# Kernel tuning notes

Hardware: AMD Instinct MI355X
Metric: run time of the kernel (lower is better)

Reference implementation:

```python
import jax, jax.numpy as jnp
import numpy as np

BLANK = 0
ALPHA = 0.25
GAMMA = 2.0
NEG = -1e30  # log-domain 'minus infinity' (finite to stay autodiff/bf16 safe)


def setup_inputs() -> dict:
    key = jax.random.key(0)
    k1, k2, k3 = jax.random.split(key, 3)
    B, T, C, S = 32, 512, 4000, 40
    tokens_btc = jax.random.normal(k1, (B, T, C), dtype=jnp.float32)
    targets_bxt = jax.random.randint(k2, (B, S), 1, C)            # labels exclude blank=0
    targets_lengths_bx1 = jax.random.randint(k3, (B,), 10, S + 1)  # per-sample target lengths
    return {
        "tokens_btc": tokens_btc,
        "targets_bxt": targets_bxt,
        "targets_lengths_bx1": targets_lengths_bx1,
    }


def _ctc_loss(log_probs_tbc, targets, target_lengths, blank):
    """Log-domain CTC forward (alpha) recursion; input lengths == T for all samples.
    Returns per-sample negative log likelihood, shape [B]."""
    T, B, C = log_probs_tbc.shape
    S = targets.shape[1]
    L = 2 * S + 1  # extended target: blank-interleaved
    ext = jnp.full((B, L), blank, dtype=targets.dtype).at[:, 1::2].set(targets)
    # skip transition (s-2 -> s) allowed iff ext[s] != blank and ext[s] != ext[s-2]
    same_as_2back = jnp.concatenate(
        [jnp.ones((B, 2), bool), ext[:, 2:] == ext[:, :-2]], axis=1)
    skip_ok = (ext != blank) & (~same_as_2back)  # [B, L]

    b_idx = jnp.arange(B)[:, None]
    lp_ext = log_probs_tbc[:, b_idx, ext]  # [T, B, L] gathered emission log-probs

    alpha0 = jnp.full((B, L), NEG, log_probs_tbc.dtype)
    alpha0 = alpha0.at[:, 0].set(lp_ext[0, :, 0]).at[:, 1].set(lp_ext[0, :, 1])

    pad1 = jnp.full((B, 1), NEG, log_probs_tbc.dtype)
    pad2 = jnp.full((B, 2), NEG, log_probs_tbc.dtype)

    def step(alpha, lp_t):
        s1 = jnp.concatenate([pad1, alpha[:, :-1]], axis=1)
        s2 = jnp.concatenate([pad2, alpha[:, :-2]], axis=1)
        a = jnp.logaddexp(alpha, s1)
        a = jnp.where(skip_ok, jnp.logaddexp(a, s2), a)
        return a + lp_t, None

    alphaT, _ = jax.lax.scan(step, alpha0, lp_ext[1:])
    end = 2 * target_lengths  # index of final blank in extended sequence
    a_last = jnp.take_along_axis(alphaT, end[:, None], axis=1)[:, 0]
    a_prev = jnp.take_along_axis(alphaT, (end - 1)[:, None], axis=1)[:, 0]
    loss = -jnp.logaddexp(a_last, a_prev)
    # zero_infinity=True: clamp infinite losses to 0
    return jnp.where(loss < 1e29, loss, 0.0)


def reference(tokens_btc, targets_bxt, targets_lengths_bx1):
    # [B,T,C] -> [T,B,C], log_softmax over classes
    log_probs_tbc = jax.nn.log_softmax(tokens_btc, axis=-1).swapaxes(0, 1)
    loss = _ctc_loss(log_probs_tbc, targets_bxt, targets_lengths_bx1, BLANK)
    # focal reweighting (alpha>0 and gamma>=0 -> enabled)
    pt = jnp.exp(-loss)
    loss = ALPHA * (1.0 - pt) ** GAMMA * loss
    return jnp.mean(loss)
```

## Files before the change

### kernel.cpp

```cpp
#include <hip/hip_runtime.h>


constexpr int B = 32;
constexpr int T = 512;
constexpr int C = 4000;
constexpr int S = 40;
constexpr int L = 2 * S + 1;
constexpr int LPS = 82;

constexpr int GATHER_BLOCKS = 1016;
constexpr int GW = GATHER_BLOCKS * 4;
constexpr int NBLK = GATHER_BLOCKS + 8;

#define NEGV -1e30f

__device__ __forceinline__ float lae(float a, float b) {
    float m = fmaxf(a, b);
    float d = fabsf(a - b);
    return m + __logf(1.0f + __expf(-d));
}

__device__ __forceinline__ float shr1_fill_neg(float x) {
    return __int_as_float(__builtin_amdgcn_update_dpp(
        __float_as_int(NEGV), __float_as_int(x),
        0x138 , 0xF, 0xF, false));
}

__global__ __launch_bounds__(256) void zero_flags_kernel(unsigned int* p, int n) {
    const int i = blockIdx.x * 256 + threadIdx.x;
    if (i < n) p[i] = 0u;
}

__global__ __launch_bounds__(256, 4) void fused_kernel(
        const float* __restrict__ tok,
        const int*   __restrict__ tgt,
        const int*   __restrict__ lens,
        float*       __restrict__ lp,
        unsigned char* __restrict__ flags,
        unsigned int* __restrict__ ctr,
        float*       __restrict__ loss_b,
        float*       __restrict__ out) {
    const int wave = threadIdx.x >> 6, lane = threadIdx.x & 63;

    if (blockIdx.x < GATHER_BLOCKS) {
        const int wg = blockIdx.x * 4 + wave;
        for (int rp = wg; rp < B * T; rp += GW) {
            const int t  = rp >> 5;
            const int bb = rp & 31;
            const int row = (bb << 9) + t;
            const size_t row_off = (size_t)row * C;
            const float4* row4 = (const float4*)(tok + row_off);

            float s = 0.0f;
            #pragma unroll
            for (int k = 0; k < 16; ++k) {
                const int i = lane + 64 * k;
                if (i < C / 4) {
                    float4 v = row4[i];
                    s += __expf(v.x) + __expf(v.y) + __expf(v.z) + __expf(v.w);
                }
            }
            #pragma unroll
            for (int off = 32; off; off >>= 1) s += __shfl_xor(s, off);
            const float lse = __logf(s);

            float* dst = lp + (size_t)row * LPS;
            {
                const int l = lane;
                int lab = 0;
                if (l & 1) lab = tgt[bb * S + (l >> 1)];
                __hip_atomic_store(dst + l, tok[row_off + lab] - lse,
                                   __ATOMIC_RELAXED, __HIP_MEMORY_SCOPE_AGENT);
            }
            if (lane < LPS - 64) {
                const int l = 64 + lane;
                float v = 0.0f;
                if (l < L) {
                    int lab = 0;
                    if (l & 1) lab = tgt[bb * S + (l >> 1)];
                    v = tok[row_off + lab] - lse;
                }
                __hip_atomic_store(dst + l, v,
                                   __ATOMIC_RELAXED, __HIP_MEMORY_SCOPE_AGENT);
            }
            asm volatile("s_waitcnt vmcnt(0)" ::: "memory");
            if (lane == 0)
                __hip_atomic_store(flags + row, (unsigned char)1,
                                   __ATOMIC_RELAXED, __HIP_MEMORY_SCOPE_AGENT);
        }
        return;
    }

    const int b  = ((blockIdx.x - GATHER_BLOCKS) << 2) + wave;
    const int ii = (lane < 41) ? lane : 40;
    const float2* base2 = (const float2*)(lp + (size_t)b * T * LPS);
    unsigned long long* fw = (unsigned long long*)(flags + ((size_t)b << 9));
    const unsigned long long ONESW = 0x0101010101010101ull;

    int ti = tgt[b * S + ((ii < 39) ? ii : 39)];
    int tp = __shfl_up(ti, 1);
    const bool skip1 = (lane >= 1) && (lane <= 39) && (ti != tp);
    const int len = lens[b];

    float a0, a1;
    auto step = [&](float2 v) {
        float p1 = shr1_fill_neg(a1);
        float m0 = fmaxf(a0, p1);
        float n0 = m0 + __logf(__expf(a0 - m0) + __expf(p1 - m0));
        float q  = skip1 ? p1 : NEGV;
        float m1 = fmaxf(fmaxf(a1, a0), q);
        float n1 = m1 + __logf(__expf(a1 - m1) + __expf(a0 - m1) + __expf(q - m1));
        a0 = n0 + v.x;
        a1 = n1 + v.y;
    };

    float2 bufA[8], bufB[8];
    unsigned long long pf = 0;

#define SPINCHUNK(c) do {                                                     \
        while (pf != ONESW)                                                   \
            pf = __hip_atomic_load(&fw[(c)], __ATOMIC_RELAXED,                \
                                   __HIP_MEMORY_SCOPE_AGENT);                 \
        __builtin_amdgcn_fence(__ATOMIC_ACQUIRE, "agent");                    \
    } while (0)
#define PREFETCHF(c) pf = ((c) < 64)                                          \
        ? __hip_atomic_load(&fw[(c)], __ATOMIC_RELAXED,                       \
                            __HIP_MEMORY_SCOPE_AGENT)                         \
        : ONESW
#define LOADCHUNK(buf, c) do { const int _t0 = (c) << 3;                      \
        _Pragma("unroll")                                                     \
        for (int _k = 0; _k < 8; ++_k)                                        \
            buf[_k] = base2[(size_t)(_t0 + _k) * 41 + ii];                    \
    } while (0)
#define STEP8(buf) do { _Pragma("unroll")                                     \
        for (int _k = 0; _k < 8; ++_k) step(buf[_k]); } while (0)

    SPINCHUNK(0); LOADCHUNK(bufA, 0);
    pf = 0; SPINCHUNK(1); LOADCHUNK(bufB, 1);
    PREFETCHF(2);

    {
        float2 v0 = bufA[0];
        a0 = (lane == 0) ? v0.x : NEGV;
        a1 = (lane == 0) ? v0.y : NEGV;
    }
    #pragma unroll
    for (int k = 1; k < 8; ++k) step(bufA[k]);

    for (int c = 1; c < 63; c += 2) {
        SPINCHUNK(c + 1); LOADCHUNK(bufA, c + 1); PREFETCHF(c + 2);
        STEP8(bufB);
        SPINCHUNK(c + 2); LOADCHUNK(bufB, c + 2); PREFETCHF(c + 3);
        STEP8(bufA);
    }
    STEP8(bufB);

    float ae = __shfl(a0, len);
    float ap = __shfl(a1, len - 1);
    if (lane == 0) {
        float loss = -lae(ae, ap);
        if (!(loss < 1e29f)) loss = 0.0f;
        float pt = __expf(-loss);
        float om = 1.0f - pt;
        __hip_atomic_store(loss_b + b, 0.25f * om * om * loss,
                           __ATOMIC_RELAXED, __HIP_MEMORY_SCOPE_AGENT);
    }
    asm volatile("s_waitcnt vmcnt(0)" ::: "memory");
    unsigned int old = 0;
    if (lane == 0)
        old = __hip_atomic_fetch_add(ctr, 1u, __ATOMIC_RELAXED,
                                     __HIP_MEMORY_SCOPE_AGENT);
    old = (unsigned int)__shfl((int)old, 0);
    if (old == B - 1) {
        __builtin_amdgcn_fence(__ATOMIC_ACQUIRE, "agent");
        float v = (lane < B) ? loss_b[lane] : 0.0f;
        #pragma unroll
        for (int off = 32; off; off >>= 1) v += __shfl_down(v, off);
        if (lane == 0) out[0] = v * (1.0f / B);
    }
#undef SPINCHUNK
#undef PREFETCHF
#undef LOADCHUNK
#undef STEP8
}

extern "C" void kernel_launch(void* const* d_in, const int* in_sizes, int n_in,
                              void* d_out, int out_size, void* d_ws, size_t ws_size,
                              hipStream_t stream) {
    const float* tok  = (const float*)d_in[0];
    const int*   tgt  = (const int*)d_in[1];
    const int*   lens = (const int*)d_in[2];
    float* out = (float*)d_out;

    float* lp = (float*)d_ws;
    unsigned char* flags = (unsigned char*)(lp + (size_t)B * T * LPS);
    unsigned int* ctr = (unsigned int*)(flags + B * T);
    float* loss_b = (float*)(flags + B * T + 64);

    zero_flags_kernel<<<17, 256, 0, stream>>>((unsigned int*)flags, 4112);
    fused_kernel<<<NBLK, 256, 0, stream>>>(tok, tgt, lens, lp, flags, ctr,
                                           loss_b, out);
}
```

Before: 407.4 us.

## Launch consumer blocks first and give each producer wave one row

The consumer (CTC recursion) blocks move to the lowest block indices so they are scheduled before the producers and can start spinning on flags right away. The producer blocks drop the grid-stride loop: each wave now handles exactly one (t,b) row, which means many more blocks are launched. Each lane also writes its blank/label pair as a single 64-bit store instead of two scalar stores. This aims to cut consumer start latency and producer store traffic, in exchange for more block launch overhead and a stray empty if-statement left in the code.

```diff
diff --git a/kernel.cpp b/kernel.cpp
--- a/kernel.cpp
+++ b/kernel.cpp
@@ -8,9 +8,9 @@
 constexpr int L = 2 * S + 1;
 constexpr int LPS = 82;
 
-constexpr int GATHER_BLOCKS = 1016;
-constexpr int GW = GATHER_BLOCKS * 4;
-constexpr int NBLK = GATHER_BLOCKS + 8;
+constexpr int CONS_BLOCKS = 8;
+constexpr int PROD_BLOCKS = B * T / 4;
+constexpr int NBLK = CONS_BLOCKS + PROD_BLOCKS;
 
 #define NEGV -1e30f
 
@@ -42,56 +42,48 @@
         float*       __restrict__ out) {
     const int wave = threadIdx.x >> 6, lane = threadIdx.x & 63;
 
-    if (blockIdx.x < GATHER_BLOCKS) {
-        const int wg = blockIdx.x * 4 + wave;
-        for (int rp = wg; rp < B * T; rp += GW) {
-            const int t  = rp >> 5;
-            const int bb = rp & 31;
-            const int row = (bb << 9) + t;
-            const size_t row_off = (size_t)row * C;
-            const float4* row4 = (const float4*)(tok + row_off);
+    if (blockIdx.x >= CONS_BLOCKS) {
+        const int rp = (blockIdx.x - CONS_BLOCKS) * 4 + wave;
+        const int t  = rp >> 5;
+        const int bb = rp & 31;
+        const int row = (bb << 9) + t;
+        const size_t row_off = (size_t)row * C;
+        const float4* row4 = (const float4*)(tok + row_off);
 
-            float s = 0.0f;
-            #pragma unroll
-            for (int k = 0; k < 16; ++k) {
-                const int i = lane + 64 * k;
-                if (i < C / 4) {
-                    float4 v = row4[i];
-                    s += __expf(v.x) + __expf(v.y) + __expf(v.z) + __expf(v.w);
-                }
+        float s = 0.0f;
+        #pragma unroll
+        for (int k = 0; k < 16; ++k) {
+            const int i = lane + 64 * k;
+            if (i < C / 4) {
+                float4 v = row4[i];
+                s += __expf(v.x) + __expf(v.y) + __expf(v.z) + __expf(v.w);
             }
-            #pragma unroll
-            for (int off = 32; off; off >>= 1) s += __shfl_xor(s, off);
-            const float lse = __logf(s);
+        }
+        #pragma unroll
+        for (int off = 32; off; off >>= 1) s += __shfl_xor(s, off);
+        const float lse = __logf(s);
 
-            float* dst = lp + (size_t)row * LPS;
-            {
-                const int l = lane;
-                int lab = 0;
-                if (l & 1) lab = tgt[bb * S + (l >> 1)];
-                __hip_atomic_store(dst + l, tok[row_off + lab] - lse,
-                                   __ATOMIC_RELAXED, __HIP_MEMORY_SCOPE_AGENT);
-            }
-            if (lane < LPS - 64) {
-                const int l = 64 + lane;
-                float v = 0.0f;
-                if (l < L) {
-                    int lab = 0;
-                    if (l & 1) lab = tgt[bb * S + (l >> 1)];
-                    v = tok[row_off + lab] - lse;
-                }
-                __hip_atomic_store(dst + l, v,
-                                   __ATOMIC_RELAXED, __HIP_MEMORY_SCOPE_AGENT);
-            }
-            asm volatile("s_waitcnt vmcnt(0)" ::: "memory");
-            if (lane == 0)
-                __hip_atomic_store(flags + row, (unsigned char)1,
-                                   __ATOMIC_RELAXED, __HIP_MEMORY_SCOPE_AGENT);
+        const float blankv = tok[row_off] - lse;
+        float labv = 0.0f;
+        if (lane >= 1 && lane <= 40)
+            ;
+        if (lane < 40)
+            labv = tok[row_off + tgt[bb * S + lane]] - lse;
+        if (lane <= 40) {
+            unsigned long long w =
+                ((unsigned long long)__float_as_uint(labv) << 32) |
+                __float_as_uint(blankv);
+            __hip_atomic_store((unsigned long long*)(lp + (size_t)row * LPS) + lane,
+                               w, __ATOMIC_RELAXED, __HIP_MEMORY_SCOPE_AGENT);
         }
+        asm volatile("s_waitcnt vmcnt(0)" ::: "memory");
+        if (lane == 0)
+            __hip_atomic_store(flags + row, (unsigned char)1,
+                               __ATOMIC_RELAXED, __HIP_MEMORY_SCOPE_AGENT);
         return;
     }
 
-    const int b  = ((blockIdx.x - GATHER_BLOCKS) << 2) + wave;
+    const int b  = blockIdx.x * 4 + wave;
     const int ii = (lane < 41) ? lane : 40;
     const float2* base2 = (const float2*)(lp + (size_t)b * T * LPS);
     unsigned long long* fw = (unsigned long long*)(flags + ((size_t)b << 9));
```

Measured after the change: 411.4 us. Within noise of the previous version (+1.0%).
